# Kernel tuning notes

Measured on AMD Instinct MI355X. Metric: run time of the kernel, lower is better.

The kernel has to match this reference:

```python
import jax, jax.numpy as jnp
import numpy as np

# Sizes
N, T, P, D = 1000, 4, 10, 13          # nodes, point types, edge types (T*(T+1)/2), basis dim per point
F, H, EA, K, E = 128, 128, 16, 64, 20000  # node feat, edge hidden, edge attr/feat, edge op bottleneck, edges
I_NODE = D * (D + 1) // 2             # 91: symmetric ('ij=ji') self-block irreps dim
I_EDGE = D * D                        # 169: generic ('ij') block irreps dim
AVG_NEIGH = 20.0


def setup_inputs() -> dict:
    ks = jax.random.split(jax.random.key(0), 16)
    Fin = H + 2 * F                   # edge-op input: [edge_msg, node_h_i, node_h_j]
    return {
        'node_feats': jax.random.normal(ks[0], (N, F), jnp.float32),
        'node_attrs': jax.random.uniform(ks[1], (N, T), dtype=jnp.float32),
        'edge_feats': jax.random.normal(ks[2], (E, EA), jnp.float32),
        'edge_attrs': jax.random.normal(ks[3], (E, EA), jnp.float32),
        'edge_index': jax.random.randint(ks[4], (2, E), 0, N),
        'node_types': jax.random.randint(ks[5], (N,), 0, T),
        'edge_types': jax.random.randint(ks[6], (E,), 0, P),
        'W_msg': jax.random.normal(ks[7], (F, F), jnp.float32) / np.float32(np.sqrt(F)),
        'W_attr': jax.random.normal(ks[8], (T, F), jnp.float32) / np.float32(np.sqrt(T)),
        'W_em': jax.random.normal(ks[9], (2 * F + 2 * EA, H), jnp.float32) / np.float32(np.sqrt(2 * F + 2 * EA)),
        'W_proj': jax.random.normal(ks[10], (Fin, K), jnp.float32) / np.float32(np.sqrt(Fin)),
        'W_node': jax.random.normal(ks[11], (T, F, I_NODE), jnp.float32) / np.float32(np.sqrt(F)),
        'W_edge': jax.random.normal(ks[12], (P, K, I_EDGE), jnp.float32) / np.float32(np.sqrt(K)),
        'cob_node': jax.random.normal(ks[13], (T, I_NODE, D, D), jnp.float32) / np.float32(D),
        'cob_edge': jax.random.normal(ks[14], (P, I_EDGE, D, D), jnp.float32) / np.float32(D),
    }


def reference(node_feats, node_attrs, edge_feats, edge_attrs, edge_index, node_types,
              edge_types, W_msg, W_attr, W_em, W_proj, W_node, W_edge, cob_node, cob_edge):
    src, dst = edge_index[0], edge_index[1]
    # --- node message passing (NodeMessageBlock, simplified linear-aggregate form) ---
    m = node_feats @ W_msg                                             # [N, F]
    agg = jax.ops.segment_sum(m[src], dst, num_segments=N) \
        + jax.ops.segment_sum(m[dst], src, num_segments=N)             # symmetric edge list: both dirs
    node_h = node_feats + agg / AVG_NEIGH + node_attrs @ W_attr        # [N, F]
    # --- edge messages (EdgeMessageBlock, simplified) ---
    e_in = jnp.concatenate([node_h[src], node_h[dst], edge_feats, edge_attrs], axis=-1)
    edge_msg = jnp.tanh(e_in @ W_em)                                   # [E, H]
    # --- self-interaction blocks: per-type gather -> op -> einsum('ni,ixy->nxy', ., cob) ---
    node_irred = jnp.einsum('nf,nfi->ni', node_h, W_node[node_types])  # [N, I_NODE]
    node_blocks = jnp.einsum('ni,nixy->nxy', node_irred, cob_node[node_types])  # [N, D, D]
    # --- interaction blocks: per-edge-type op + change of basis, transpose-symmetrized ---
    onehot = jax.nn.one_hot(edge_types, P, dtype=node_feats.dtype)     # [E, P] type selector

    def edge_block(a, b):
        h = jnp.concatenate([edge_msg, a, b], axis=-1) @ W_proj        # [E, K]
        irr = jnp.einsum('epi,ep->ei', jnp.einsum('ek,pki->epi', h, W_edge), onehot)  # [E, I_EDGE]
        return jnp.einsum('epxy,ep->exy', jnp.einsum('ei,pixy->epxy', irr, cob_edge), onehot)  # [E, D, D]

    blk_ij = edge_block(node_h[src], node_h[dst])
    blk_ji = edge_block(node_h[dst], node_h[src])
    edge_blocks = 0.5 * (blk_ij + jnp.swapaxes(blk_ji, -1, -2))        # symm_transpose
    # --- scatter blocks into the dense symmetric block matrix ---
    off = jnp.arange(D)
    nidx = jnp.arange(N)[:, None] * D + off                            # [N, D] diagonal block rows/cols
    rs = src[:, None] * D + off                                        # [E, D]
    cs = dst[:, None] * D + off
    M = jnp.zeros((N * D, N * D), node_feats.dtype)
    M = M.at[nidx[:, :, None], nidx[:, None, :]].add(node_blocks)
    M = M.at[rs[:, :, None], cs[:, None, :]].add(edge_blocks)
    M = M.at[cs[:, :, None], rs[:, None, :]].add(jnp.swapaxes(edge_blocks, -1, -2))
    return M
```

## Files before the change

### kernel.cpp

```cpp
#include <hip/hip_runtime.h>
#include <cmath>

#define NN   1000
#define TT   4
#define PP   10
#define DD   13
#define FF   128
#define HH   128
#define EAA  16
#define KDIM 64
#define EE   20000
#define I_NODE 91
#define I_EDGE 169
#define MROW  13000

__global__ __launch_bounds__(256) void k_zero(float4* __restrict__ p, long n4) {
  long i = (long)blockIdx.x * 256 + threadIdx.x;
  if (i < n4) p[i] = make_float4(0.f, 0.f, 0.f, 0.f);
}

__global__ __launch_bounds__(192) void k_comb_edge(
    const float* __restrict__ We, const float* __restrict__ cob,
    float* __restrict__ Wcomb) {
  int pk = blockIdx.x;
  int p = pk >> 6;
  int t = threadIdx.x;
  if (t >= I_EDGE) return;
  float acc = 0.f;
  const float* wrow = We + pk * I_EDGE;
  const float* crow = cob + p * I_EDGE * I_EDGE + t;
  for (int i = 0; i < I_EDGE; ++i) acc += wrow[i] * crow[i * I_EDGE];
  Wcomb[pk * I_EDGE + t] = acc;
}

__global__ __launch_bounds__(192) void k_comb_node(
    const float* __restrict__ Wn, const float* __restrict__ cob,
    float* __restrict__ Wnc) {
  int tf = blockIdx.x;
  int ty = tf >> 7;
  int t = threadIdx.x;
  if (t >= I_EDGE) return;
  float acc = 0.f;
  const float* wrow = Wn + tf * I_NODE;
  const float* crow = cob + ty * I_NODE * I_EDGE + t;
  for (int i = 0; i < I_NODE; ++i) acc += wrow[i] * crow[i * I_EDGE];
  Wnc[tf * I_EDGE + t] = acc;
}

__global__ __launch_bounds__(128) void k_node_msg(
    const float* __restrict__ nf, const float* __restrict__ Wmsg,
    float* __restrict__ m, float* __restrict__ agg) {
  int n = blockIdx.x, j = threadIdx.x;
  __shared__ float row[FF];
  row[j] = nf[n * FF + j];
  __syncthreads();
  float acc = 0.f;
#pragma unroll 8
  for (int f = 0; f < FF; ++f) acc += row[f] * Wmsg[f * FF + j];
  m[n * FF + j] = acc;
  agg[n * FF + j] = 0.f;
}

__global__ __launch_bounds__(256) void k_scatter(
    const float* __restrict__ m, const int* __restrict__ src,
    const int* __restrict__ dst, float* __restrict__ agg) {
  int idx = blockIdx.x * 256 + threadIdx.x;
  if (idx >= EE * FF) return;
  int e = idx >> 7, j = idx & 127;
  int s = src[e], d = dst[e];
  atomicAdd(&agg[d * FF + j], m[s * FF + j]);
  atomicAdd(&agg[s * FF + j], m[d * FF + j]);
}

__global__ __launch_bounds__(128) void k_node_h(
    const float* __restrict__ nf, const float* __restrict__ agg,
    const float* __restrict__ na, const float* __restrict__ Wattr,
    float* __restrict__ nh) {
  int n = blockIdx.x, j = threadIdx.x;
  float a = 0.f;
#pragma unroll
  for (int t = 0; t < TT; ++t) a += na[n * TT + t] * Wattr[t * FF + j];
  nh[n * FF + j] = nf[n * FF + j] + agg[n * FF + j] * (1.0f / 20.0f) + a;
}

#define EPB 8
__global__ __launch_bounds__(128) void k_edge_msg(
    const float* __restrict__ nh, const float* __restrict__ ef,
    const float* __restrict__ ea, const int* __restrict__ src,
    const int* __restrict__ dst, const float* __restrict__ Wem,
    float* __restrict__ emsg) {
  int e0 = blockIdx.x * EPB;
  int j = threadIdx.x;
  __shared__ float xin[EPB][2 * FF + 2 * EAA];
  for (int e = 0; e < EPB; ++e) {
    int ee = e0 + e;
    int s = src[ee], d = dst[ee];
    for (int i = j; i < 288; i += 128) {
      float v;
      if (i < 128)      v = nh[s * FF + i];
      else if (i < 256) v = nh[d * FF + (i - 128)];
      else if (i < 272) v = ef[ee * EAA + (i - 256)];
      else              v = ea[ee * EAA + (i - 272)];
      xin[e][i] = v;
    }
  }
  __syncthreads();
  float acc[EPB];
#pragma unroll
  for (int e = 0; e < EPB; ++e) acc[e] = 0.f;
  for (int c = 0; c < 288; c += 4) {
    float4 xv[EPB];
#pragma unroll
    for (int e = 0; e < EPB; ++e) xv[e] = *(const float4*)&xin[e][c];
#pragma unroll
    for (int sub = 0; sub < 4; ++sub) {
      float w = Wem[(c + sub) * HH + j];
      const float* xs;
#pragma unroll
      for (int e = 0; e < EPB; ++e) {
        float x = (sub == 0) ? xv[e].x : (sub == 1) ? xv[e].y : (sub == 2) ? xv[e].z : xv[e].w;
        acc[e] += x * w;
      }
    }
  }
#pragma unroll
  for (int e = 0; e < EPB; ++e) emsg[(e0 + e) * HH + j] = tanhf(acc[e]);
}

__global__ __launch_bounds__(192) void k_node_block(
    const float* __restrict__ nh, const int* __restrict__ ntype,
    const float* __restrict__ Wnc, float* __restrict__ M) {
  int n = blockIdx.x, t = threadIdx.x;
  int ty = ntype[n];
  __shared__ float row[FF];
  if (t < FF) row[t] = nh[n * FF + t];
  __syncthreads();
  if (t < I_EDGE) {
    float acc = 0.f;
    const float* W = Wnc + ty * FF * I_EDGE + t;
#pragma unroll 4
    for (int f = 0; f < FF; ++f) acc += row[f] * W[f * I_EDGE];
    int x = t / DD, y = t % DD;
    atomicAdd(&M[(size_t)(n * DD + x) * MROW + (n * DD + y)], acc);
  }
}

#define E2 2
__global__ __launch_bounds__(256) void k_edge_blk(
    const float* __restrict__ nh, const float* __restrict__ emsg,
    const int* __restrict__ src, const int* __restrict__ dst,
    const int* __restrict__ etype, const float* __restrict__ Wproj,
    const float* __restrict__ Wcomb, float* __restrict__ M) {
  int e0 = blockIdx.x * E2;
  int t = threadIdx.x;
  __shared__ float xin[E2][384];
  __shared__ float hp[4][256];
  __shared__ float hv[4][KDIM];
  __shared__ float tji[E2][I_EDGE];
  __shared__ int se[E2], de[E2], pe[E2];

  if (t < E2) {
    int e = e0 + t;
    se[t] = src[e]; de[t] = dst[e]; pe[t] = etype[e];
  }
  __syncthreads();
  for (int e = 0; e < E2; ++e) {
    int ee = e0 + e, s = se[e], d = de[e];
    if (t < 128) {
      xin[e][t] = emsg[ee * HH + t];
      xin[e][256 + t] = nh[d * FF + t];
    } else {
      xin[e][t] = nh[s * FF + (t - 128)];
    }
  }
  __syncthreads();

  {
    int k = t & 63, seg = t >> 6;
    float a0 = 0.f, a1 = 0.f, a2 = 0.f, a3 = 0.f;
    const float* Wp = Wproj + k;
    int i0 = seg * 96;
    for (int c = i0; c < i0 + 96; c += 4) {
      int cs = (c < 128) ? c : (c < 256 ? c + 128 : c - 128);
      float4 x0 = *(const float4*)&xin[0][c];
      float4 x0s = *(const float4*)&xin[0][cs];
      float4 x1 = *(const float4*)&xin[1][c];
      float4 x1s = *(const float4*)&xin[1][cs];
      float w0 = Wp[(c + 0) * KDIM], w1 = Wp[(c + 1) * KDIM];
      float w2 = Wp[(c + 2) * KDIM], w3 = Wp[(c + 3) * KDIM];
      a0 += x0.x * w0 + x0.y * w1 + x0.z * w2 + x0.w * w3;
      a1 += x0s.x * w0 + x0s.y * w1 + x0s.z * w2 + x0s.w * w3;
      a2 += x1.x * w0 + x1.y * w1 + x1.z * w2 + x1.w * w3;
      a3 += x1s.x * w0 + x1s.y * w1 + x1s.z * w2 + x1s.w * w3;
    }
    hp[0][t] = a0; hp[1][t] = a1; hp[2][t] = a2; hp[3][t] = a3;
  }
  __syncthreads();
  if (t < KDIM) {
#pragma unroll
    for (int q = 0; q < 4; ++q)
      hv[q][t] = hp[q][t] + hp[q][t + 64] + hp[q][t + 128] + hp[q][t + 192];
  }
  __syncthreads();

  float b0 = 0.f, b1 = 0.f, b2 = 0.f, b3 = 0.f;
  if (t < I_EDGE) {
    const float* W0 = Wcomb + pe[0] * KDIM * I_EDGE + t;
    const float* W1 = Wcomb + pe[1] * KDIM * I_EDGE + t;
    for (int k = 0; k < KDIM; k += 4) {
      float4 h0 = *(const float4*)&hv[0][k];
      float4 h1 = *(const float4*)&hv[1][k];
      float4 h2 = *(const float4*)&hv[2][k];
      float4 h3 = *(const float4*)&hv[3][k];
      float u0 = W0[(k + 0) * I_EDGE], u1 = W0[(k + 1) * I_EDGE];
      float u2 = W0[(k + 2) * I_EDGE], u3 = W0[(k + 3) * I_EDGE];
      float v0 = W1[(k + 0) * I_EDGE], v1 = W1[(k + 1) * I_EDGE];
      float v2 = W1[(k + 2) * I_EDGE], v3 = W1[(k + 3) * I_EDGE];
      b0 += h0.x * u0 + h0.y * u1 + h0.z * u2 + h0.w * u3;
      b1 += h1.x * u0 + h1.y * u1 + h1.z * u2 + h1.w * u3;
      b2 += h2.x * v0 + h2.y * v1 + h2.z * v2 + h2.w * v3;
      b3 += h3.x * v0 + h3.y * v1 + h3.z * v2 + h3.w * v3;
    }
    tji[0][t] = b1; tji[1][t] = b3;
  }
  __syncthreads();

  if (t < I_EDGE) {
    int x = t / DD, y = t % DD;
    {
      int s = se[0], d = de[0];
      float eb = 0.5f * (b0 + tji[0][y * DD + x]);
      atomicAdd(&M[(size_t)(s * DD + x) * MROW + (d * DD + y)], eb);
      atomicAdd(&M[(size_t)(d * DD + y) * MROW + (s * DD + x)], eb);
    }
    {
      int s = se[1], d = de[1];
      float eb = 0.5f * (b2 + tji[1][y * DD + x]);
      atomicAdd(&M[(size_t)(s * DD + x) * MROW + (d * DD + y)], eb);
      atomicAdd(&M[(size_t)(d * DD + y) * MROW + (s * DD + x)], eb);
    }
  }
}

extern "C" void kernel_launch(void* const* d_in, const int* in_sizes, int n_in,
                              void* d_out, int out_size, void* d_ws, size_t ws_size,
                              hipStream_t stream) {
  const float* node_feats = (const float*)d_in[0];
  const float* node_attrs = (const float*)d_in[1];
  const float* edge_feats = (const float*)d_in[2];
  const float* edge_attrs = (const float*)d_in[3];
  const int*   edge_index = (const int*)d_in[4];
  const int*   node_types = (const int*)d_in[5];
  const int*   edge_types = (const int*)d_in[6];
  const float* W_msg  = (const float*)d_in[7];
  const float* W_attr = (const float*)d_in[8];
  const float* W_em   = (const float*)d_in[9];
  const float* W_proj = (const float*)d_in[10];
  const float* W_node = (const float*)d_in[11];
  const float* W_edge = (const float*)d_in[12];
  const float* cob_node = (const float*)d_in[13];
  const float* cob_edge = (const float*)d_in[14];

  float* M  = (float*)d_out;
  float* ws = (float*)d_ws;
  float* m_buf = ws;
  float* agg   = ws + 128000;
  float* nh    = ws + 256000;
  float* emsg  = ws + 384000;
  float* Wcomb = ws + 2944000;
  float* Wnc   = ws + 3052160;

  const int* src = edge_index;
  const int* dst = edge_index + EE;

  long n4 = (long)out_size / 4;
  k_zero      <<<(int)((n4 + 255) / 256), 256, 0, stream>>>((float4*)M, n4);
  k_comb_edge <<<PP * KDIM, 192, 0, stream>>>(W_edge, cob_edge, Wcomb);
  k_comb_node <<<TT * FF, 192, 0, stream>>>(W_node, cob_node, Wnc);
  k_node_msg  <<<NN, 128, 0, stream>>>(node_feats, W_msg, m_buf, agg);
  k_scatter   <<<(EE * FF) / 256, 256, 0, stream>>>(m_buf, src, dst, agg);
  k_node_h    <<<NN, 128, 0, stream>>>(node_feats, agg, node_attrs, W_attr, nh);
  k_edge_msg  <<<EE / EPB, 128, 0, stream>>>(nh, edge_feats, edge_attrs, src, dst, W_em, emsg);
  k_node_block<<<NN, 192, 0, stream>>>(nh, node_types, Wnc, M);
  k_edge_blk  <<<EE / E2, 256, 0, stream>>>(nh, emsg, src, dst, edge_types,
                                            W_proj, Wcomb, M);
}
```

Before: 919.9 us.

## Replace atomic scatters with CSR-style neighbor lists and per-node bucketed block writes

```diff
diff --git a/kernel.cpp b/kernel.cpp
--- a/kernel.cpp
+++ b/kernel.cpp
@@ -13,10 +13,21 @@
 #define I_NODE 91
 #define I_EDGE 169
 #define MROW  13000
-
-__global__ __launch_bounds__(256) void k_zero(float4* __restrict__ p, long n4) {
-  long i = (long)blockIdx.x * 256 + threadIdx.x;
-  if (i < n4) p[i] = make_float4(0.f, 0.f, 0.f, 0.f);
+#define NCAP 192
+#define BCAP 256
+
+typedef float floatx4 __attribute__((ext_vector_type(4)));
+
+__global__ __launch_bounds__(256) void k_zero(floatx4* __restrict__ p, long n4) {
+  long stride = (long)gridDim.x * 256;
+  floatx4 z = (floatx4)(0.f);
+  for (long i = (long)blockIdx.x * 256 + threadIdx.x; i < n4; i += stride)
+    __builtin_nontemporal_store(z, &p[i]);
+}
+
+__global__ void k_setup(int* __restrict__ curN, int* __restrict__ cntA) {
+  int i = blockIdx.x * 256 + threadIdx.x;
+  if (i < NN) { curN[i] = 0; cntA[i] = 0; }
 }
 
 __global__ __launch_bounds__(192) void k_comb_edge(
@@ -49,7 +60,7 @@
 
 __global__ __launch_bounds__(128) void k_node_msg(
     const float* __restrict__ nf, const float* __restrict__ Wmsg,
-    float* __restrict__ m, float* __restrict__ agg) {
+    float* __restrict__ m) {
   int n = blockIdx.x, j = threadIdx.x;
   __shared__ float row[FF];
   row[j] = nf[n * FF + j];
@@ -58,29 +69,34 @@
 #pragma unroll 8
   for (int f = 0; f < FF; ++f) acc += row[f] * Wmsg[f * FF + j];
   m[n * FF + j] = acc;
-  agg[n * FF + j] = 0.f;
-}
-
-__global__ __launch_bounds__(256) void k_scatter(
-    const float* __restrict__ m, const int* __restrict__ src,
-    const int* __restrict__ dst, float* __restrict__ agg) {
-  int idx = blockIdx.x * 256 + threadIdx.x;
-  if (idx >= EE * FF) return;
-  int e = idx >> 7, j = idx & 127;
+}
+
+__global__ __launch_bounds__(256) void k_build(
+    const int* __restrict__ src, const int* __restrict__ dst,
+    int* __restrict__ curN, int* __restrict__ nbrs,
+    int* __restrict__ cntA, int* __restrict__ bucketA) {
+  int e = blockIdx.x * 256 + threadIdx.x;
+  if (e >= EE) return;
   int s = src[e], d = dst[e];
-  atomicAdd(&agg[d * FF + j], m[s * FF + j]);
-  atomicAdd(&agg[s * FF + j], m[d * FF + j]);
+  int ps = atomicAdd(&curN[s], 1); if (ps < NCAP) nbrs[s * NCAP + ps] = d;
+  int pd = atomicAdd(&curN[d], 1); if (pd < NCAP) nbrs[d * NCAP + pd] = s;
+  int a = (s < d) ? s : d;
+  int pa = atomicAdd(&cntA[a], 1); if (pa < BCAP) bucketA[a * BCAP + pa] = e;
 }
 
 __global__ __launch_bounds__(128) void k_node_h(
-    const float* __restrict__ nf, const float* __restrict__ agg,
+    const float* __restrict__ nf, const float* __restrict__ m,
     const float* __restrict__ na, const float* __restrict__ Wattr,
+    const int* __restrict__ curN, const int* __restrict__ nbrs,
     float* __restrict__ nh) {
   int n = blockIdx.x, j = threadIdx.x;
+  int deg = curN[n]; if (deg > NCAP) deg = NCAP;
+  float acc = 0.f;
+  for (int l = 0; l < deg; ++l) acc += m[nbrs[n * NCAP + l] * FF + j];
   float a = 0.f;
 #pragma unroll
   for (int t = 0; t < TT; ++t) a += na[n * TT + t] * Wattr[t * FF + j];
-  nh[n * FF + j] = nf[n * FF + j] + agg[n * FF + j] * (1.0f / 20.0f) + a;
+  nh[n * FF + j] = nf[n * FF + j] + acc * (1.0f / 20.0f) + a;
 }
 
 #define EPB 8
@@ -115,7 +131,6 @@
 #pragma unroll
     for (int sub = 0; sub < 4; ++sub) {
       float w = Wem[(c + sub) * HH + j];
-      const float* xs;
 #pragma unroll
       for (int e = 0; e < EPB; ++e) {
         float x = (sub == 0) ? xv[e].x : (sub == 1) ? xv[e].y : (sub == 2) ? xv[e].z : xv[e].w;
@@ -141,7 +156,7 @@
 #pragma unroll 4
     for (int f = 0; f < FF; ++f) acc += row[f] * W[f * I_EDGE];
     int x = t / DD, y = t % DD;
-    atomicAdd(&M[(size_t)(n * DD + x) * MROW + (n * DD + y)], acc);
+    M[(size_t)(n * DD + x) * MROW + (n * DD + y)] = acc;
   }
 }
 
@@ -150,7 +165,7 @@
     const float* __restrict__ nh, const float* __restrict__ emsg,
     const int* __restrict__ src, const int* __restrict__ dst,
     const int* __restrict__ etype, const float* __restrict__ Wproj,
-    const float* __restrict__ Wcomb, float* __restrict__ M) {
+    const float* __restrict__ Wcomb, float* __restrict__ eb) {
   int e0 = blockIdx.x * E2;
   int t = threadIdx.x;
   __shared__ float xin[E2][384];
@@ -227,17 +242,53 @@
 
   if (t < I_EDGE) {
     int x = t / DD, y = t % DD;
-    {
-      int s = se[0], d = de[0];
-      float eb = 0.5f * (b0 + tji[0][y * DD + x]);
-      atomicAdd(&M[(size_t)(s * DD + x) * MROW + (d * DD + y)], eb);
-      atomicAdd(&M[(size_t)(d * DD + y) * MROW + (s * DD + x)], eb);
-    }
-    {
-      int s = se[1], d = de[1];
-      float eb = 0.5f * (b2 + tji[1][y * DD + x]);
-      atomicAdd(&M[(size_t)(s * DD + x) * MROW + (d * DD + y)], eb);
-      atomicAdd(&M[(size_t)(d * DD + y) * MROW + (s * DD + x)], eb);
+    int tr = y * DD + x;
+    eb[(size_t)(e0 + 0) * I_EDGE + t] = 0.5f * (b0 + tji[0][tr]);
+    eb[(size_t)(e0 + 1) * I_EDGE + t] = 0.5f * (b2 + tji[1][tr]);
+  }
+}
+
+__global__ __launch_bounds__(192) void k_write(
+    const float* __restrict__ eb, const int* __restrict__ src,
+    const int* __restrict__ dst, const int* __restrict__ cntA,
+    const int* __restrict__ bucketA, float* __restrict__ M) {
+  int a = blockIdx.x, t = threadIdx.x;
+  int na = cntA[a]; if (na > BCAP) na = BCAP;
+  if (na == 0) return;
+  __shared__ int bL[BCAP];
+  __shared__ int eidL[BCAP];
+  __shared__ int flipL[BCAP];
+  for (int i = t; i < na; i += 192) {
+    int e = bucketA[a * BCAP + i];
+    int s = src[e], d = dst[e];
+    bL[i] = s + d - a;
+    eidL[i] = e;
+    flipL[i] = (s != a);
+  }
+  __syncthreads();
+  if (t >= I_EDGE) return;
+  int x = t / DD, y = t % DD;
+  int tr = y * DD + x;
+  for (int i = 0; i < na; ++i) {
+    int b = bL[i];
+    bool owner = true;
+    for (int j = 0; j < i; ++j)
+      if (bL[j] == b) { owner = false; break; }
+    if (!owner) continue;
+    float acc_ab = 0.f, acc_ba = 0.f;
+    for (int j = i; j < na; ++j) {
+      if (bL[j] != b) continue;
+      const float* ebp = eb + (size_t)eidL[j] * I_EDGE;
+      float vt = ebp[t], vr = ebp[tr];
+      if (!flipL[j]) { acc_ab += vt; acc_ba += vr; }
+      else           { acc_ab += vr; acc_ba += vt; }
+    }
+    if (b == a) {
+      size_t idx = (size_t)(a * DD + x) * MROW + a * DD + y;
+      M[idx] += acc_ab + acc_ba;
+    } else {
+      M[(size_t)(a * DD + x) * MROW + b * DD + y] = acc_ab;
+      M[(size_t)(b * DD + x) * MROW + a * DD + y] = acc_ba;
     }
   }
 }
@@ -264,24 +315,30 @@
   float* M  = (float*)d_out;
   float* ws = (float*)d_ws;
   float* m_buf = ws;
-  float* agg   = ws + 128000;
-  float* nh    = ws + 256000;
-  float* emsg  = ws + 384000;
-  float* Wcomb = ws + 2944000;
-  float* Wnc   = ws + 3052160;
+  float* nh    = ws + 128000;
+  float* emsg  = ws + 256000;
+  float* eb    = ws + 2816000;
+  float* Wcomb = ws + 6196000;
+  float* Wnc   = ws + 6304160;
+  int*   ibase   = (int*)(ws + 6390688);
+  int*   curN    = ibase;
+  int*   cntA    = ibase + 1000;
+  int*   nbrs    = ibase + 2000;
+  int*   bucketA = ibase + 194000;
 
   const int* src = edge_index;
   const int* dst = edge_index + EE;
 
   long n4 = (long)out_size / 4;
-  k_zero      <<<(int)((n4 + 255) / 256), 256, 0, stream>>>((float4*)M, n4);
+  k_zero      <<<8192, 256, 0, stream>>>((floatx4*)M, n4);
+  k_setup     <<<(NN + 255) / 256, 256, 0, stream>>>(curN, cntA);
   k_comb_edge <<<PP * KDIM, 192, 0, stream>>>(W_edge, cob_edge, Wcomb);
   k_comb_node <<<TT * FF, 192, 0, stream>>>(W_node, cob_node, Wnc);
-  k_node_msg  <<<NN, 128, 0, stream>>>(node_feats, W_msg, m_buf, agg);
-  k_scatter   <<<(EE * FF) / 256, 256, 0, stream>>>(m_buf, src, dst, agg);
-  k_node_h    <<<NN, 128, 0, stream>>>(node_feats, agg, node_attrs, W_attr, nh);
+  k_node_msg  <<<NN, 128, 0, stream>>>(node_feats, W_msg, m_buf);
+  k_build     <<<(EE + 255) / 256, 256, 0, stream>>>(src, dst, curN, nbrs, cntA, bucketA);
+  k_node_h    <<<NN, 128, 0, stream>>>(node_feats, m_buf, node_attrs, W_attr, curN, nbrs, nh);
   k_edge_msg  <<<EE / EPB, 128, 0, stream>>>(nh, edge_feats, edge_attrs, src, dst, W_em, emsg);
   k_node_block<<<NN, 192, 0, stream>>>(nh, node_types, Wnc, M);
-  k_edge_blk  <<<EE / E2, 256, 0, stream>>>(nh, emsg, src, dst, edge_types,
-                                            W_proj, Wcomb, M);
-}
+  k_edge_blk  <<<EE / E2, 256, 0, stream>>>(nh, emsg, src, dst, edge_types, W_proj, Wcomb, eb);
+  k_write     <<<NN, 192, 0, stream>>>(eb, src, dst, cntA, bucketA, M);
+}
```

Result: slower. 1.144 ms (+24.4%).
